# Kernel optimization log

Measured on AMD Instinct MI355X. Metric: run time of the kernel, lower is better.

Reference implementation:

```python
import jax, jax.numpy as jnp
import numpy as np

E, T, K, H, I = 16, 512, 8, 2048, 1024  # experts, tokens, top-k, hidden, ffn half-width


def setup_inputs() -> dict:
    key = jax.random.key(0)
    ks = jax.random.split(key, 8)
    x = jax.random.normal(ks[0], (T, H), dtype=jnp.float32)
    expert_ids = jax.random.randint(ks[1], (T, K), 0, E, dtype=jnp.int32)
    # int8-valued weights stored as int32 (exactly representable)
    gmm1_weight = jax.random.randint(ks[2], (E, H, 2 * I), -127, 128, dtype=jnp.int32)
    gmm2_weight = jax.random.randint(ks[3], (E, I, H), -127, 128, dtype=jnp.int32)
    gmm1_weight_scale = jax.random.uniform(ks[4], (E, 2 * I), dtype=jnp.float32) * 1e-3
    gmm2_weight_scale = jax.random.uniform(ks[5], (E, H), dtype=jnp.float32) * 1e-3
    smooth_scales = jax.random.uniform(ks[6], (E, H), dtype=jnp.float32)
    expert_scales = jax.random.uniform(ks[7], (T, K), dtype=jnp.float32)
    return {"x": x, "expert_ids": expert_ids, "gmm1_weight": gmm1_weight,
            "gmm1_weight_scale": gmm1_weight_scale, "gmm2_weight": gmm2_weight,
            "gmm2_weight_scale": gmm2_weight_scale, "smooth_scales": smooth_scales,
            "expert_scales": expert_scales}


def _dynamic_quant(v):
    # per-token symmetric dynamic quant to int8 range (quant_mode=2 / quant_mode=1)
    s = jnp.max(jnp.abs(v), axis=-1, keepdims=True) / 127.0
    q = jnp.clip(jnp.round(v / s), -128.0, 127.0)  # kept in f32; values are exact small ints
    return q, s


def _grouped_mm(a, w, e_flat):
    # grouped GEMM: out[i] = a[i] @ w[e_flat[i]]. Disjoint expert masks -> masked full GEMMs summed.
    out = jnp.zeros((a.shape[0], w.shape[-1]), dtype=a.dtype)
    for e in range(w.shape[0]):
        mask = (e_flat == e)[:, None]
        out = out + jnp.where(mask, a, 0.0) @ w[e]
    return out


def reference(x, expert_ids, gmm1_weight, gmm1_weight_scale, gmm2_weight,
              gmm2_weight_scale, smooth_scales, expert_scales):
    # --- dispatch: per-token dynamic int8 quant + replicate each token K times ---
    xq, s0 = _dynamic_quant(x)                 # [T,H], [T,1]
    e_flat = expert_ids.reshape(-1)            # [T*K]
    xq_e = jnp.repeat(xq, K, axis=0)           # [T*K,H]
    s0_e = jnp.repeat(s0, K, axis=0)           # [T*K,1] == dynamic_scales / activation_scale
    w1 = gmm1_weight.astype(jnp.float32)       # int8 GEMM emulated exactly in f32
    w2 = gmm2_weight.astype(jnp.float32)
    # --- grouped GEMM 1 -> int32 accumulator values ---
    y1_i32 = _grouped_mm(xq_e, w1, e_flat)     # [T*K,2I]
    # --- fused dequant + SwiGLU (activate_left) + per-token dynamic requant ---
    y1f = y1_i32 * gmm1_weight_scale[e_flat] * s0_e
    act = jax.nn.silu(y1f[:, :I]) * y1f[:, I:]
    aq, s1 = _dynamic_quant(act)               # [T*K,I], [T*K,1]
    # --- grouped GEMM 2 + dequant (per-channel weight scale * per-token scale) ---
    y2_i32 = _grouped_mm(aq, w2, e_flat)       # [T*K,H]
    y2 = y2_i32 * gmm2_weight_scale[e_flat] * s1
    # --- combine: weighted sum over the K expert copies of each token ---
    out = jnp.einsum('tkh,tk->th', y2.reshape(T, K, H), expert_scales)
    return out
```

## Files before the change

kernel.cpp:

```cpp
#include <hip/hip_runtime.h>
#include <hip/hip_bf16.h>
#include <stdint.h>

#define E_   16
#define T_   512
#define KTOP 8
#define H_   2048
#define I_   1024
#define TK_  4096

typedef __attribute__((ext_vector_type(4))) int i32x4;

#define OFF_CNT     0
#define OFF_ROWMAX  4096
#define OFF_XQ      32768
#define OFF_S0      (OFF_XQ + T_*H_)
#define OFF_S1      (OFF_S0 + 4096)
#define OFF_LIST    (OFF_S1 + TK_*4)
#define OFF_ACT     (OFF_LIST + E_*TK_*4)
#define OFF_AQ      (OFF_ACT + (size_t)TK_*I_*4)
#define OFF_Y2      (OFF_AQ + (size_t)TK_*I_)

__device__ __forceinline__ void g2l16(const void* g, void* l) {
  __builtin_amdgcn_global_load_lds(
      (const __attribute__((address_space(1))) void*)g,
      (__attribute__((address_space(3))) void*)l, 16, 0, 0);
}

#define SCHEDB() __builtin_amdgcn_sched_barrier(0)
#define VMCNT16() asm volatile("s_waitcnt vmcnt(16)" ::: "memory")
#define VMCNT0()  asm volatile("s_waitcnt vmcnt(0)" ::: "memory")
#define LGKM0()   asm volatile("s_waitcnt lgkmcnt(0)" ::: "memory")
#define BAR()     __builtin_amdgcn_s_barrier()

__global__ void k_zero(unsigned int* __restrict__ p) {
  int i = blockIdx.x * 256 + threadIdx.x;
  if (i < 5120) p[i] = 0;
}

__global__ void k_quant(const float* __restrict__ x, signed char* __restrict__ xq,
                        float* __restrict__ s0, const int* __restrict__ eids,
                        unsigned int* __restrict__ counts, int* __restrict__ row_list) {
  int t = blockIdx.x, tid = threadIdx.x;
  if (tid < KTOP) {
    int e = eids[t * KTOP + tid];
    int pos = (int)atomicAdd(&counts[e], 1u);
    row_list[e * TK_ + pos] = t * KTOP + tid;
  }
  const float4* xr = (const float4*)(x + (size_t)t * H_);
  float4 a = xr[tid * 2 + 0], b = xr[tid * 2 + 1];
  float m = fmaxf(
      fmaxf(fmaxf(fabsf(a.x), fabsf(a.y)), fmaxf(fabsf(a.z), fabsf(a.w))),
      fmaxf(fmaxf(fabsf(b.x), fabsf(b.y)), fmaxf(fabsf(b.z), fabsf(b.w))));
  for (int o = 32; o > 0; o >>= 1) m = fmaxf(m, __shfl_xor(m, o));
  __shared__ float wm[4];
  if ((tid & 63) == 0) wm[tid >> 6] = m;
  __syncthreads();
  m = fmaxf(fmaxf(wm[0], wm[1]), fmaxf(wm[2], wm[3]));
  float s = m / 127.0f;
  if (!(s > 0.f)) s = 1.0f;
  if (tid == 0) s0[t] = s;
  float v[8] = {a.x, a.y, a.z, a.w, b.x, b.y, b.z, b.w};
  unsigned int lo = 0, hi = 0;
#pragma unroll
  for (int j = 0; j < 4; ++j) {
    float qf = fminf(fmaxf(rintf(v[j] / s), -128.f), 127.f);
    lo |= ((unsigned)((int)qf & 0xFF)) << (8 * j);
  }
#pragma unroll
  for (int j = 0; j < 4; ++j) {
    float qf = fminf(fmaxf(rintf(v[4 + j] / s), -128.f), 127.f);
    hi |= ((unsigned)((int)qf & 0xFF)) << (8 * j);
  }
  ((uint2*)(xq + (size_t)t * H_))[tid] = make_uint2(lo, hi);
}

#define BM_   320
#define ABUF  20480
#define BBUF  4096
#define WSTR  2048

#define PACKW(SRC, DST) do {                                              \
    i32x4 pk_;                                                            \
    _Pragma("unroll")                                                     \
    for (int d_ = 0; d_ < 4; ++d_)                                        \
      pk_[d_] = ((SRC)[4*d_] & 0xFF) | (((SRC)[4*d_+1] & 0xFF) << 8) |    \
                (((SRC)[4*d_+2] & 0xFF) << 16) | ((SRC)[4*d_+3] << 24);   \
    *(i32x4*)(DST) = pk_;                                                 \
  } while (0)

#define TILE_BODY(TT, RD, PK, IS, LAST, NT) do {                          \
    if (!(LAST)) {                                                        \
      _Pragma("unroll")                                                   \
      for (int i_ = 0; i_ < 5; ++i_)                                      \
        g2l16(gA[i_] + ((TT) + 1) * 64,                                   \
              smem + ((RD) ^ 1) * ABUF + (w * 5 + i_) * 1024);            \
    }                                                                     \
    SCHEDB();                                                             \
    {                                                                     \
      int kk_ = (TT) + 2; if (kk_ > (NT) - 1) kk_ = (NT) - 1;             \
      _Pragma("unroll")                                                   \
      for (int j_ = 0; j_ < 16; ++j_)                                     \
        (IS)[j_] = bsrc[(size_t)(kk_ * 64 + j_) * WSTR];                  \
    }                                                                     \
    SCHEDB();                                                             \
    {                                                                     \
      const char* Ab_ = smem + (RD) * ABUF;                               \
      const char* Bb_ = smem + 2 * ABUF + (RD) * BBUF;                    \
      i32x4 af_[5], bf_[4];                                               \
      _Pragma("unroll")                                                   \
      for (int i_ = 0; i_ < 5; ++i_)                                      \
        af_[i_] = *(const i32x4*)(Ab_ + (w * 5 + i_) * 1024 + lane * 16); \
      _Pragma("unroll")                                                   \
      for (int n_ = 0; n_ < 4; ++n_)                                      \
        bf_[n_] = *(const i32x4*)(Bb_ + l4 * 1024 + (n_ * 16 + l15) * 16);\
      _Pragma("unroll")                                                   \
      for (int i_ = 0; i_ < 5; ++i_)                                      \
        _Pragma("unroll")                                                 \
        for (int n_ = 0; n_ < 4; ++n_)                                    \
          acc[i_][n_] = __builtin_amdgcn_mfma_i32_16x16x64_i8(            \
              af_[i_], bf_[n_], acc[i_][n_], 0, 0, 0);                    \
    }                                                                     \
    if (!(LAST)) {                                                        \
      VMCNT16(); SCHEDB();                                                \
      PACKW(PK, bdst0 + (((RD) ^ 1)) * BBUF);                             \
      LGKM0(); BAR(); SCHEDB();                                           \
    }                                                                     \
  } while (0)

__launch_bounds__(256, 2)
__global__ void k_gemm1(const signed char* __restrict__ xq, const int* __restrict__ w1,
                        const float* __restrict__ ws1, const float* __restrict__ s0,
                        const unsigned int* __restrict__ counts,
                        const int* __restrict__ row_list,
                        float* __restrict__ act, unsigned int* __restrict__ rowmax) {
  __shared__ alignas(16) char smem[2 * ABUF + 2 * BBUF];
  int e = blockIdx.y;
  int cnt = (int)counts[e];
  if (cnt == 0) return;
  int p0 = blockIdx.x * 32;
  const int* rl = row_list + e * TK_;
  const int* we = w1 + (size_t)e * H_ * (2 * I_);
  const float* wsc = ws1 + (size_t)e * (2 * I_);

  int tid = threadIdx.x, w = tid >> 6, lane = tid & 63;
  int l15 = lane & 15, l4 = lane >> 4;
  int bc = tid & 63, bkg = tid >> 6;
  int bgcol = (bc < 32) ? (p0 + bc) : (I_ + p0 + (bc - 32));
  const int* bsrc = we + (size_t)(bkg * 16) * WSTR + bgcol;
  char* bdst0 = smem + 2 * ABUF + bkg * 1024 + bc * 16;

  const int NT = H_ / 64;
  int nch = (cnt + BM_ - 1) / BM_;
  for (int ch = 0; ch < nch; ++ch) {
    int rbase = ch * BM_;
    const signed char* gA[5];
#pragma unroll
    for (int i = 0; i < 5; ++i) {
      int gr = rbase + w * 80 + i * 16 + l15;
      int tok = rl[gr < cnt ? gr : 0] >> 3;
      gA[i] = xq + (size_t)tok * H_ + l4 * 16;
    }
    i32x4 acc[5][4];
#pragma unroll
    for (int i = 0; i < 5; ++i)
#pragma unroll
      for (int n = 0; n < 4; ++n) acc[i][n] = (i32x4)(0);

    int brA[16], brB[16];
    SCHEDB();
#pragma unroll
    for (int i = 0; i < 5; ++i) g2l16(gA[i], smem + (w * 5 + i) * 1024);
    SCHEDB();
#pragma unroll
    for (int j = 0; j < 16; ++j) brA[j] = bsrc[(size_t)j * WSTR];
    SCHEDB();
#pragma unroll
    for (int j = 0; j < 16; ++j) brB[j] = bsrc[(size_t)(64 + j) * WSTR];
    SCHEDB();
    VMCNT16(); SCHEDB();
    PACKW(brA, bdst0);
    LGKM0(); BAR(); SCHEDB();

    for (int t = 0; t < NT; t += 2) {
      TILE_BODY(t,     0, brB, brA, false,          NT);
      TILE_BODY(t + 1, 1, brA, brB, (t + 2 == NT),  NT);
    }

#pragma unroll
    for (int mi = 0; mi < 5; ++mi) {
#pragma unroll
      for (int r = 0; r < 4; ++r) {
        int gr = rbase + w * 80 + mi * 16 + l4 * 4 + r;
        bool valid = gr < cnt;
        int irow = rl[valid ? gr : 0];
        float s0v = s0[irow >> 3];
        float rowm = 0.f, av0 = 0.f, av1 = 0.f;
#pragma unroll
        for (int n = 0; n < 2; ++n) {
          int colL = p0 + n * 16 + l15;
          float yl = (float)acc[mi][n][r] * wsc[colL] * s0v;
          float yr = (float)acc[mi][n + 2][r] * wsc[I_ + colL] * s0v;
          float actv = (yl / (1.f + expf(-yl))) * yr;
          if (n == 0) av0 = actv; else av1 = actv;
          rowm = fmaxf(rowm, fabsf(actv));
        }
        rowm = fmaxf(rowm, __shfl_xor(rowm, 1));
        rowm = fmaxf(rowm, __shfl_xor(rowm, 2));
        rowm = fmaxf(rowm, __shfl_xor(rowm, 4));
        rowm = fmaxf(rowm, __shfl_xor(rowm, 8));
        if (valid) {
          act[(size_t)irow * I_ + p0 + l15] = av0;
          act[(size_t)irow * I_ + p0 + 16 + l15] = av1;
          if (l15 == 0) atomicMax(rowmax + irow, __float_as_uint(rowm));
        }
      }
    }
  }
}

__global__ void k_requant(const float* __restrict__ act, const unsigned int* __restrict__ rowmax,
                          signed char* __restrict__ aq, float* __restrict__ s1) {
  int i = blockIdx.x, tid = threadIdx.x;
  float m = __uint_as_float(rowmax[i]);
  float s = (m > 0.f) ? (m / 127.0f) : 1.0f;
  if (tid == 0) s1[i] = s;
  float4 v = ((const float4*)(act + (size_t)i * I_))[tid];
  float vv[4] = {v.x, v.y, v.z, v.w};
  unsigned int pk = 0;
#pragma unroll
  for (int j = 0; j < 4; ++j) {
    float qf = fminf(fmaxf(rintf(vv[j] / s), -128.f), 127.f);
    pk |= ((unsigned)((int)qf & 0xFF)) << (8 * j);
  }
  ((unsigned int*)(aq + (size_t)i * I_))[tid] = pk;
}

__launch_bounds__(256, 2)
__global__ void k_gemm2(const signed char* __restrict__ aq, const int* __restrict__ w2,
                        const float* __restrict__ ws2, const float* __restrict__ s1,
                        const float* __restrict__ es,
                        const unsigned int* __restrict__ counts,
                        const int* __restrict__ row_list,
                        __hip_bfloat16* __restrict__ y2h) {
  __shared__ alignas(16) char smem[2 * ABUF + 2 * BBUF];
  int e = blockIdx.y;
  int cnt = (int)counts[e];
  if (cnt == 0) return;
  int n0 = blockIdx.x * 64;
  const int* rl = row_list + e * TK_;
  const int* we = w2 + (size_t)e * I_ * H_;
  const float* wsc = ws2 + (size_t)e * H_;

  int tid = threadIdx.x, w = tid >> 6, lane = tid & 63;
  int l15 = lane & 15, l4 = lane >> 4;
  int bc = tid & 63, bkg = tid >> 6;
  const int* bsrc = we + (size_t)(bkg * 16) * WSTR + n0 + bc;
  char* bdst0 = smem + 2 * ABUF + bkg * 1024 + bc * 16;

  const int NT = I_ / 64;
  int nch = (cnt + BM_ - 1) / BM_;
  for (int ch = 0; ch < nch; ++ch) {
    int rbase = ch * BM_;
    const signed char* gA[5];
#pragma unroll
    for (int i = 0; i < 5; ++i) {
      int gr = rbase + w * 80 + i * 16 + l15;
      gA[i] = aq + (size_t)rl[gr < cnt ? gr : 0] * I_ + l4 * 16;
    }
    i32x4 acc[5][4];
#pragma unroll
    for (int i = 0; i < 5; ++i)
#pragma unroll
      for (int n = 0; n < 4; ++n) acc[i][n] = (i32x4)(0);

    int brA[16], brB[16];
    SCHEDB();
#pragma unroll
    for (int i = 0; i < 5; ++i) g2l16(gA[i], smem + (w * 5 + i) * 1024);
    SCHEDB();
#pragma unroll
    for (int j = 0; j < 16; ++j) brA[j] = bsrc[(size_t)j * WSTR];
    SCHEDB();
#pragma unroll
    for (int j = 0; j < 16; ++j) brB[j] = bsrc[(size_t)(64 + j) * WSTR];
    SCHEDB();
    VMCNT16(); SCHEDB();
    PACKW(brA, bdst0);
    LGKM0(); BAR(); SCHEDB();

    for (int t = 0; t < NT; t += 2) {
      TILE_BODY(t,     0, brB, brA, false,          NT);
      TILE_BODY(t + 1, 1, brA, brB, (t + 2 == NT),  NT);
    }

#pragma unroll
    for (int mi = 0; mi < 5; ++mi) {
#pragma unroll
      for (int r = 0; r < 4; ++r) {
        int gr = rbase + w * 80 + mi * 16 + l4 * 4 + r;
        if (gr < cnt) {
          int irow = rl[gr];
          float sc = s1[irow] * es[irow];
#pragma unroll
          for (int n = 0; n < 4; ++n) {
            int col = n0 + n * 16 + l15;
            float v = (float)acc[mi][n][r] * wsc[col] * sc;
            y2h[(size_t)irow * H_ + col] = __float2bfloat16(v);
          }
        }
      }
    }
  }
}

__global__ void k_combine(const __hip_bfloat16* __restrict__ y2h, float* __restrict__ out) {
  int idx = blockIdx.x * 256 + threadIdx.x;
  int t = idx >> 8;
  int h0 = (idx & 255) * 8;
  float s[8];
#pragma unroll
  for (int j = 0; j < 8; ++j) s[j] = 0.f;
#pragma unroll
  for (int k = 0; k < KTOP; ++k) {
    const __hip_bfloat16* p = y2h + ((size_t)(t * KTOP + k) * H_ + h0);
    uint4 u = *(const uint4*)p;
    const __hip_bfloat16* b = (const __hip_bfloat16*)&u;
#pragma unroll
    for (int j = 0; j < 8; ++j) s[j] += __bfloat162float(b[j]);
  }
  float4 o0 = make_float4(s[0], s[1], s[2], s[3]);
  float4 o1 = make_float4(s[4], s[5], s[6], s[7]);
  float4* dst = (float4*)(out + (size_t)t * H_ + h0);
  dst[0] = o0; dst[1] = o1;
}

extern "C" void kernel_launch(void* const* d_in, const int* in_sizes, int n_in,
                              void* d_out, int out_size, void* d_ws, size_t ws_size,
                              hipStream_t stream) {
  const float* x   = (const float*)d_in[0];
  const int*   eid = (const int*)d_in[1];
  const int*   w1  = (const int*)d_in[2];
  const float* ws1 = (const float*)d_in[3];
  const int*   w2  = (const int*)d_in[4];
  const float* ws2 = (const float*)d_in[5];
  const float* es  = (const float*)d_in[7];
  float* out = (float*)d_out;
  char* ws = (char*)d_ws;

  unsigned int*  counts   = (unsigned int*)(ws + OFF_CNT);
  unsigned int*  rowmax   = (unsigned int*)(ws + OFF_ROWMAX);
  signed char*   xq       = (signed char*)(ws + OFF_XQ);
  float*         s0       = (float*)(ws + OFF_S0);
  float*         s1       = (float*)(ws + OFF_S1);
  int*           row_list = (int*)(ws + OFF_LIST);
  float*         act      = (float*)(ws + OFF_ACT);
  signed char*   aq       = (signed char*)(ws + OFF_AQ);
  __hip_bfloat16* y2h     = (__hip_bfloat16*)(ws + OFF_Y2);

  k_zero<<<20, 256, 0, stream>>>((unsigned int*)ws);
  k_quant<<<T_, 256, 0, stream>>>(x, xq, s0, eid, counts, row_list);
  k_gemm1<<<dim3(32, E_), 256, 0, stream>>>(xq, w1, ws1, s0, counts, row_list, act, rowmax);
  k_requant<<<TK_, 256, 0, stream>>>(act, rowmax, aq, s1);
  k_gemm2<<<dim3(32, E_), 256, 0, stream>>>(aq, w2, ws2, s1, es, counts, row_list, y2h);
  k_combine<<<(T_ * H_ / 8) / 256, 256, 0, stream>>>(y2h, out);
}
```

Baseline: 178.2 us.

## Replace LDS-staged GEMM blocks with single-wave register-pipelined tiles over more blocks

Both grouped GEMM kernels drop the 256-thread LDS double-buffered design. They now use 64-thread single-wave blocks that load A and B fragments straight into registers with a two-stage register double buffer. The grid gains a third dimension that splits row chunks across 5 blocks, and each block covers a narrower column strip (16+16 columns for gemm1, 32 for gemm2), giving many more blocks to fill the GPU. The cost is weaker reuse: each weight column strip is reloaded by more blocks, B is fetched with strided scalar int32 loads per wave, and there is no shared-memory sharing.

```diff
diff --git a/kernel.cpp b/kernel.cpp
--- a/kernel.cpp
+++ b/kernel.cpp
@@ -20,18 +20,6 @@
 #define OFF_ACT     (OFF_LIST + E_*TK_*4)
 #define OFF_AQ      (OFF_ACT + (size_t)TK_*I_*4)
 #define OFF_Y2      (OFF_AQ + (size_t)TK_*I_)
-
-__device__ __forceinline__ void g2l16(const void* g, void* l) {
-  __builtin_amdgcn_global_load_lds(
-      (const __attribute__((address_space(1))) void*)g,
-      (__attribute__((address_space(3))) void*)l, 16, 0, 0);
-}
-
-#define SCHEDB() __builtin_amdgcn_sched_barrier(0)
-#define VMCNT16() asm volatile("s_waitcnt vmcnt(16)" ::: "memory")
-#define VMCNT0()  asm volatile("s_waitcnt vmcnt(0)" ::: "memory")
-#define LGKM0()   asm volatile("s_waitcnt lgkmcnt(0)" ::: "memory")
-#define BAR()     __builtin_amdgcn_s_barrier()
 
 __global__ void k_zero(unsigned int* __restrict__ p) {
   int i = blockIdx.x * 256 + threadIdx.x;
@@ -75,143 +63,105 @@
   ((uint2*)(xq + (size_t)t * H_))[tid] = make_uint2(lo, hi);
 }
 
-#define BM_   320
-#define ABUF  20480
-#define BBUF  4096
-#define WSTR  2048
-
-#define PACKW(SRC, DST) do {                                              \
-    i32x4 pk_;                                                            \
+__device__ __forceinline__ i32x4 packb(const int* s) {
+  i32x4 r;
+#pragma unroll
+  for (int d = 0; d < 4; ++d)
+    r[d] = (s[4 * d] & 0xFF) | ((s[4 * d + 1] & 0xFF) << 8) |
+           ((s[4 * d + 2] & 0xFF) << 16) | (s[4 * d + 3] << 24);
+  return r;
+}
+
+#define LOADA(BANK, TT)                                                   \
+  _Pragma("unroll")                                                       \
+  for (int i_ = 0; i_ < 5; ++i_)                                          \
+    BANK[i_] = *(const i32x4*)(gA[i_] + (TT) * 64);
+
+#define LOADB(BL, BR, TT)                                                 \
+  _Pragma("unroll")                                                       \
+  for (int j_ = 0; j_ < 16; ++j_) {                                       \
+    BL[j_] = weL[(size_t)((TT) * 64 + j_) * 2048];                        \
+    BR[j_] = weR[(size_t)((TT) * 64 + j_) * 2048];                        \
+  }
+
+#define COMP(AB, BL, BR)                                                  \
+  do {                                                                    \
+    i32x4 fL_ = packb(BL), fR_ = packb(BR);                               \
     _Pragma("unroll")                                                     \
-    for (int d_ = 0; d_ < 4; ++d_)                                        \
-      pk_[d_] = ((SRC)[4*d_] & 0xFF) | (((SRC)[4*d_+1] & 0xFF) << 8) |    \
-                (((SRC)[4*d_+2] & 0xFF) << 16) | ((SRC)[4*d_+3] << 24);   \
-    *(i32x4*)(DST) = pk_;                                                 \
-  } while (0)
-
-#define TILE_BODY(TT, RD, PK, IS, LAST, NT) do {                          \
-    if (!(LAST)) {                                                        \
-      _Pragma("unroll")                                                   \
-      for (int i_ = 0; i_ < 5; ++i_)                                      \
-        g2l16(gA[i_] + ((TT) + 1) * 64,                                   \
-              smem + ((RD) ^ 1) * ABUF + (w * 5 + i_) * 1024);            \
-    }                                                                     \
-    SCHEDB();                                                             \
-    {                                                                     \
-      int kk_ = (TT) + 2; if (kk_ > (NT) - 1) kk_ = (NT) - 1;             \
-      _Pragma("unroll")                                                   \
-      for (int j_ = 0; j_ < 16; ++j_)                                     \
-        (IS)[j_] = bsrc[(size_t)(kk_ * 64 + j_) * WSTR];                  \
-    }                                                                     \
-    SCHEDB();                                                             \
-    {                                                                     \
-      const char* Ab_ = smem + (RD) * ABUF;                               \
-      const char* Bb_ = smem + 2 * ABUF + (RD) * BBUF;                    \
-      i32x4 af_[5], bf_[4];                                               \
-      _Pragma("unroll")                                                   \
-      for (int i_ = 0; i_ < 5; ++i_)                                      \
-        af_[i_] = *(const i32x4*)(Ab_ + (w * 5 + i_) * 1024 + lane * 16); \
-      _Pragma("unroll")                                                   \
-      for (int n_ = 0; n_ < 4; ++n_)                                      \
-        bf_[n_] = *(const i32x4*)(Bb_ + l4 * 1024 + (n_ * 16 + l15) * 16);\
-      _Pragma("unroll")                                                   \
-      for (int i_ = 0; i_ < 5; ++i_)                                      \
-        _Pragma("unroll")                                                 \
-        for (int n_ = 0; n_ < 4; ++n_)                                    \
-          acc[i_][n_] = __builtin_amdgcn_mfma_i32_16x16x64_i8(            \
-              af_[i_], bf_[n_], acc[i_][n_], 0, 0, 0);                    \
-    }                                                                     \
-    if (!(LAST)) {                                                        \
-      VMCNT16(); SCHEDB();                                                \
-      PACKW(PK, bdst0 + (((RD) ^ 1)) * BBUF);                             \
-      LGKM0(); BAR(); SCHEDB();                                           \
+    for (int i_ = 0; i_ < 5; ++i_) {                                      \
+      acc[i_][0] = __builtin_amdgcn_mfma_i32_16x16x64_i8(                 \
+          AB[i_], fL_, acc[i_][0], 0, 0, 0);                              \
+      acc[i_][1] = __builtin_amdgcn_mfma_i32_16x16x64_i8(                 \
+          AB[i_], fR_, acc[i_][1], 0, 0, 0);                              \
     }                                                                     \
   } while (0)
 
-__launch_bounds__(256, 2)
+__launch_bounds__(64, 2)
 __global__ void k_gemm1(const signed char* __restrict__ xq, const int* __restrict__ w1,
                         const float* __restrict__ ws1, const float* __restrict__ s0,
                         const unsigned int* __restrict__ counts,
                         const int* __restrict__ row_list,
                         float* __restrict__ act, unsigned int* __restrict__ rowmax) {
-  __shared__ alignas(16) char smem[2 * ABUF + 2 * BBUF];
+  int strip = blockIdx.x;
   int e = blockIdx.y;
   int cnt = (int)counts[e];
-  if (cnt == 0) return;
-  int p0 = blockIdx.x * 32;
+  int p0 = strip * 16;
   const int* rl = row_list + e * TK_;
   const int* we = w1 + (size_t)e * H_ * (2 * I_);
   const float* wsc = ws1 + (size_t)e * (2 * I_);
 
-  int tid = threadIdx.x, w = tid >> 6, lane = tid & 63;
+  int lane = threadIdx.x & 63;
   int l15 = lane & 15, l4 = lane >> 4;
-  int bc = tid & 63, bkg = tid >> 6;
-  int bgcol = (bc < 32) ? (p0 + bc) : (I_ + p0 + (bc - 32));
-  const int* bsrc = we + (size_t)(bkg * 16) * WSTR + bgcol;
-  char* bdst0 = smem + 2 * ABUF + bkg * 1024 + bc * 16;
-
-  const int NT = H_ / 64;
-  int nch = (cnt + BM_ - 1) / BM_;
-  for (int ch = 0; ch < nch; ++ch) {
-    int rbase = ch * BM_;
+
+  const int* weL = we + (size_t)(l4 * 16) * 2048 + p0 + l15;
+  const int* weR = weL + I_;
+
+  for (int ch = blockIdx.z; ch * 80 < cnt; ch += 5) {
+    int rbase = ch * 80;
     const signed char* gA[5];
 #pragma unroll
     for (int i = 0; i < 5; ++i) {
-      int gr = rbase + w * 80 + i * 16 + l15;
+      int gr = rbase + i * 16 + l15;
       int tok = rl[gr < cnt ? gr : 0] >> 3;
       gA[i] = xq + (size_t)tok * H_ + l4 * 16;
     }
-    i32x4 acc[5][4];
-#pragma unroll
-    for (int i = 0; i < 5; ++i)
-#pragma unroll
-      for (int n = 0; n < 4; ++n) acc[i][n] = (i32x4)(0);
-
-    int brA[16], brB[16];
-    SCHEDB();
-#pragma unroll
-    for (int i = 0; i < 5; ++i) g2l16(gA[i], smem + (w * 5 + i) * 1024);
-    SCHEDB();
-#pragma unroll
-    for (int j = 0; j < 16; ++j) brA[j] = bsrc[(size_t)j * WSTR];
-    SCHEDB();
-#pragma unroll
-    for (int j = 0; j < 16; ++j) brB[j] = bsrc[(size_t)(64 + j) * WSTR];
-    SCHEDB();
-    VMCNT16(); SCHEDB();
-    PACKW(brA, bdst0);
-    LGKM0(); BAR(); SCHEDB();
-
-    for (int t = 0; t < NT; t += 2) {
-      TILE_BODY(t,     0, brB, brA, false,          NT);
-      TILE_BODY(t + 1, 1, brA, brB, (t + 2 == NT),  NT);
+    i32x4 acc[5][2];
+#pragma unroll
+    for (int i = 0; i < 5; ++i) { acc[i][0] = (i32x4)(0); acc[i][1] = (i32x4)(0); }
+
+    i32x4 a0[5], a1[5];
+    int b0L[16], b0R[16], b1L[16], b1R[16];
+
+    LOADA(a0, 0);
+    LOADB(b0L, b0R, 0);
+    for (int t = 0; t < 32; t += 2) {
+      LOADA(a1, t + 1);
+      LOADB(b1L, b1R, t + 1);
+      COMP(a0, b0L, b0R);
+      int p2 = (t + 2 < 32) ? (t + 2) : t;
+      LOADA(a0, p2);
+      LOADB(b0L, b0R, p2);
+      COMP(a1, b1L, b1R);
     }
 
 #pragma unroll
     for (int mi = 0; mi < 5; ++mi) {
 #pragma unroll
       for (int r = 0; r < 4; ++r) {
-        int gr = rbase + w * 80 + mi * 16 + l4 * 4 + r;
+        int gr = rbase + mi * 16 + l4 * 4 + r;
         bool valid = gr < cnt;
         int irow = rl[valid ? gr : 0];
         float s0v = s0[irow >> 3];
-        float rowm = 0.f, av0 = 0.f, av1 = 0.f;
-#pragma unroll
-        for (int n = 0; n < 2; ++n) {
-          int colL = p0 + n * 16 + l15;
-          float yl = (float)acc[mi][n][r] * wsc[colL] * s0v;
-          float yr = (float)acc[mi][n + 2][r] * wsc[I_ + colL] * s0v;
-          float actv = (yl / (1.f + expf(-yl))) * yr;
-          if (n == 0) av0 = actv; else av1 = actv;
-          rowm = fmaxf(rowm, fabsf(actv));
-        }
+        float yl = (float)acc[mi][0][r] * wsc[p0 + l15] * s0v;
+        float yr = (float)acc[mi][1][r] * wsc[I_ + p0 + l15] * s0v;
+        float actv = (yl / (1.f + expf(-yl))) * yr;
+        float rowm = fabsf(actv);
         rowm = fmaxf(rowm, __shfl_xor(rowm, 1));
         rowm = fmaxf(rowm, __shfl_xor(rowm, 2));
         rowm = fmaxf(rowm, __shfl_xor(rowm, 4));
         rowm = fmaxf(rowm, __shfl_xor(rowm, 8));
         if (valid) {
-          act[(size_t)irow * I_ + p0 + l15] = av0;
-          act[(size_t)irow * I_ + p0 + 16 + l15] = av1;
+          act[(size_t)irow * I_ + p0 + l15] = actv;
           if (l15 == 0) atomicMax(rowmax + irow, __float_as_uint(rowm));
         }
       }
@@ -236,77 +186,67 @@
   ((unsigned int*)(aq + (size_t)i * I_))[tid] = pk;
 }
 
-__launch_bounds__(256, 2)
+__launch_bounds__(64, 2)
 __global__ void k_gemm2(const signed char* __restrict__ aq, const int* __restrict__ w2,
                         const float* __restrict__ ws2, const float* __restrict__ s1,
                         const float* __restrict__ es,
                         const unsigned int* __restrict__ counts,
                         const int* __restrict__ row_list,
                         __hip_bfloat16* __restrict__ y2h) {
-  __shared__ alignas(16) char smem[2 * ABUF + 2 * BBUF];
+  int strip = blockIdx.x;
   int e = blockIdx.y;
   int cnt = (int)counts[e];
-  if (cnt == 0) return;
-  int n0 = blockIdx.x * 64;
+  int n0 = strip * 32;
   const int* rl = row_list + e * TK_;
   const int* we = w2 + (size_t)e * I_ * H_;
   const float* wsc = ws2 + (size_t)e * H_;
 
-  int tid = threadIdx.x, w = tid >> 6, lane = tid & 63;
+  int lane = threadIdx.x & 63;
   int l15 = lane & 15, l4 = lane >> 4;
-  int bc = tid & 63, bkg = tid >> 6;
-  const int* bsrc = we + (size_t)(bkg * 16) * WSTR + n0 + bc;
-  char* bdst0 = smem + 2 * ABUF + bkg * 1024 + bc * 16;
-
-  const int NT = I_ / 64;
-  int nch = (cnt + BM_ - 1) / BM_;
-  for (int ch = 0; ch < nch; ++ch) {
-    int rbase = ch * BM_;
+
+  const int* weL = we + (size_t)(l4 * 16) * 2048 + n0 + l15;
+  const int* weR = weL + 16;
+
+  for (int ch = blockIdx.z; ch * 80 < cnt; ch += 5) {
+    int rbase = ch * 80;
     const signed char* gA[5];
 #pragma unroll
     for (int i = 0; i < 5; ++i) {
-      int gr = rbase + w * 80 + i * 16 + l15;
+      int gr = rbase + i * 16 + l15;
       gA[i] = aq + (size_t)rl[gr < cnt ? gr : 0] * I_ + l4 * 16;
     }
-    i32x4 acc[5][4];
-#pragma unroll
-    for (int i = 0; i < 5; ++i)
-#pragma unroll
-      for (int n = 0; n < 4; ++n) acc[i][n] = (i32x4)(0);
-
-    int brA[16], brB[16];
-    SCHEDB();
-#pragma unroll
-    for (int i = 0; i < 5; ++i) g2l16(gA[i], smem + (w * 5 + i) * 1024);
-    SCHEDB();
-#pragma unroll
-    for (int j = 0; j < 16; ++j) brA[j] = bsrc[(size_t)j * WSTR];
-    SCHEDB();
-#pragma unroll
-    for (int j = 0; j < 16; ++j) brB[j] = bsrc[(size_t)(64 + j) * WSTR];
-    SCHEDB();
-    VMCNT16(); SCHEDB();
-    PACKW(brA, bdst0);
-    LGKM0(); BAR(); SCHEDB();
-
-    for (int t = 0; t < NT; t += 2) {
-      TILE_BODY(t,     0, brB, brA, false,          NT);
-      TILE_BODY(t + 1, 1, brA, brB, (t + 2 == NT),  NT);
+    i32x4 acc[5][2];
+#pragma unroll
+    for (int i = 0; i < 5; ++i) { acc[i][0] = (i32x4)(0); acc[i][1] = (i32x4)(0); }
+
+    i32x4 a0[5], a1[5];
+    int b0L[16], b0R[16], b1L[16], b1R[16];
+
+    LOADA(a0, 0);
+    LOADB(b0L, b0R, 0);
+    for (int t = 0; t < 16; t += 2) {
+      LOADA(a1, t + 1);
+      LOADB(b1L, b1R, t + 1);
+      COMP(a0, b0L, b0R);
+      int p2 = (t + 2 < 16) ? (t + 2) : t;
+      LOADA(a0, p2);
+      LOADB(b0L, b0R, p2);
+      COMP(a1, b1L, b1R);
     }
 
 #pragma unroll
     for (int mi = 0; mi < 5; ++mi) {
 #pragma unroll
       for (int r = 0; r < 4; ++r) {
-        int gr = rbase + w * 80 + mi * 16 + l4 * 4 + r;
+        int gr = rbase + mi * 16 + l4 * 4 + r;
         if (gr < cnt) {
           int irow = rl[gr];
           float sc = s1[irow] * es[irow];
 #pragma unroll
-          for (int n = 0; n < 4; ++n) {
-            int col = n0 + n * 16 + l15;
-            float v = (float)acc[mi][n][r] * wsc[col] * sc;
-            y2h[(size_t)irow * H_ + col] = __float2bfloat16(v);
+          for (int n = 0; n < 2; ++n) {
+            int c = n0 + n * 16 + l15;
+            float v = (float)acc[mi][n][r] * wsc[c] * sc;
+            y2h[(size_t)irow * H_ + c] = __float2bfloat16(v);
           }
         }
       }
@@ -360,8 +300,8 @@
 
   k_zero<<<20, 256, 0, stream>>>((unsigned int*)ws);
   k_quant<<<T_, 256, 0, stream>>>(x, xq, s0, eid, counts, row_list);
-  k_gemm1<<<dim3(32, E_), 256, 0, stream>>>(xq, w1, ws1, s0, counts, row_list, act, rowmax);
+  k_gemm1<<<dim3(64, E_, 5), 64, 0, stream>>>(xq, w1, ws1, s0, counts, row_list, act, rowmax);
   k_requant<<<TK_, 256, 0, stream>>>(act, rowmax, aq, s1);
-  k_gemm2<<<dim3(32, E_), 256, 0, stream>>>(aq, w2, ws2, s1, es, counts, row_list, y2h);
+  k_gemm2<<<dim3(64, E_, 5), 64, 0, stream>>>(aq, w2, ws2, s1, es, counts, row_list, y2h);
   k_combine<<<(T_ * H_ / 8) / 256, 256, 0, stream>>>(y2h, out);
 }
```

After: 456.4 us. 2.56x slower.

## Load A tiles directly into registers, stage only B through LDS

Applied to the files above, without the earlier changes.

Both grouped GEMM kernels now load the activation (A) fragments straight from global memory into registers, double-buffered across k-tiles, instead of staging them through LDS with global_load_lds. Only the packed weight (B) tile still goes through a small double-buffered LDS area, which cuts shared memory per block from about 48KB to 8KB. This removes the LDS write/read round trip for A. In exchange it adds register pressure from the extra A and B register banks, makes global A loads lane-gathered rather than LDS-mediated, and needs a barrier between row chunks.

```diff
diff --git a/kernel.cpp b/kernel.cpp
--- a/kernel.cpp
+++ b/kernel.cpp
@@ -21,15 +21,8 @@
 #define OFF_AQ      (OFF_ACT + (size_t)TK_*I_*4)
 #define OFF_Y2      (OFF_AQ + (size_t)TK_*I_)
 
-__device__ __forceinline__ void g2l16(const void* g, void* l) {
-  __builtin_amdgcn_global_load_lds(
-      (const __attribute__((address_space(1))) void*)g,
-      (__attribute__((address_space(3))) void*)l, 16, 0, 0);
-}
-
 #define SCHEDB() __builtin_amdgcn_sched_barrier(0)
-#define VMCNT16() asm volatile("s_waitcnt vmcnt(16)" ::: "memory")
-#define VMCNT0()  asm volatile("s_waitcnt vmcnt(0)" ::: "memory")
+#define VMCNT26() asm volatile("s_waitcnt vmcnt(26)" ::: "memory")
 #define LGKM0()   asm volatile("s_waitcnt lgkmcnt(0)" ::: "memory")
 #define BAR()     __builtin_amdgcn_s_barrier()
 
@@ -76,8 +69,6 @@
 }
 
 #define BM_   320
-#define ABUF  20480
-#define BBUF  4096
 #define WSTR  2048
 
 #define PACKW(SRC, DST) do {                                              \
@@ -89,41 +80,39 @@
     *(i32x4*)(DST) = pk_;                                                 \
   } while (0)
 
-#define TILE_BODY(TT, RD, PK, IS, LAST, NT) do {                          \
-    if (!(LAST)) {                                                        \
+#define LOADB(BANK, TT)                                                   \
+    _Pragma("unroll")                                                     \
+    for (int j_ = 0; j_ < 16; ++j_)                                       \
+      BANK[j_] = bsrc[(size_t)((TT) * 64 + j_) * WSTR];
+
+#define LOADAR(BANK, TT)                                                  \
+    _Pragma("unroll")                                                     \
+    for (int i_ = 0; i_ < 5; ++i_)                                        \
+      BANK[i_] = *(const i32x4*)(gA[i_] + (TT) * 64);
+
+#define MFMAS(ABANK, P)                                                   \
+    _Pragma("unroll")                                                     \
+    for (int n_ = 0; n_ < 4; ++n_) {                                      \
+      i32x4 bf_ = *(const i32x4*)(bsm + (P) * 4096 + l4 * 1024 +          \
+                                  (n_ * 16 + l15) * 16);                  \
       _Pragma("unroll")                                                   \
       for (int i_ = 0; i_ < 5; ++i_)                                      \
-        g2l16(gA[i_] + ((TT) + 1) * 64,                                   \
-              smem + ((RD) ^ 1) * ABUF + (w * 5 + i_) * 1024);            \
-    }                                                                     \
+        acc[i_][n_] = __builtin_amdgcn_mfma_i32_16x16x64_i8(              \
+            ABANK[i_], bf_, acc[i_][n_], 0, 0, 0);                        \
+    }
+
+#define TILE(TT, P, ABANK, BBANK, PKBANK, NT, LAST) do {                  \
+    int tn_ = (TT) + 2; if (tn_ > (NT) - 1) tn_ = (NT) - 1;               \
     SCHEDB();                                                             \
-    {                                                                     \
-      int kk_ = (TT) + 2; if (kk_ > (NT) - 1) kk_ = (NT) - 1;             \
-      _Pragma("unroll")                                                   \
-      for (int j_ = 0; j_ < 16; ++j_)                                     \
-        (IS)[j_] = bsrc[(size_t)(kk_ * 64 + j_) * WSTR];                  \
-    }                                                                     \
+    LOADB(BBANK, tn_);                                                    \
     SCHEDB();                                                             \
-    {                                                                     \
-      const char* Ab_ = smem + (RD) * ABUF;                               \
-      const char* Bb_ = smem + 2 * ABUF + (RD) * BBUF;                    \
-      i32x4 af_[5], bf_[4];                                               \
-      _Pragma("unroll")                                                   \
-      for (int i_ = 0; i_ < 5; ++i_)                                      \
-        af_[i_] = *(const i32x4*)(Ab_ + (w * 5 + i_) * 1024 + lane * 16); \
-      _Pragma("unroll")                                                   \
-      for (int n_ = 0; n_ < 4; ++n_)                                      \
-        bf_[n_] = *(const i32x4*)(Bb_ + l4 * 1024 + (n_ * 16 + l15) * 16);\
-      _Pragma("unroll")                                                   \
-      for (int i_ = 0; i_ < 5; ++i_)                                      \
-        _Pragma("unroll")                                                 \
-        for (int n_ = 0; n_ < 4; ++n_)                                    \
-          acc[i_][n_] = __builtin_amdgcn_mfma_i32_16x16x64_i8(            \
-              af_[i_], bf_[n_], acc[i_][n_], 0, 0, 0);                    \
-    }                                                                     \
+    MFMAS(ABANK, P);                                                      \
+    SCHEDB();                                                             \
+    LOADAR(ABANK, tn_);                                                   \
+    SCHEDB();                                                             \
     if (!(LAST)) {                                                        \
-      VMCNT16(); SCHEDB();                                                \
-      PACKW(PK, bdst0 + (((RD) ^ 1)) * BBUF);                             \
+      VMCNT26(); SCHEDB();                                                \
+      PACKW(PKBANK, bsm + ((P) ^ 1) * 4096 + bkg * 1024 + bc * 16);       \
       LGKM0(); BAR(); SCHEDB();                                           \
     }                                                                     \
   } while (0)
@@ -134,7 +123,7 @@
                         const unsigned int* __restrict__ counts,
                         const int* __restrict__ row_list,
                         float* __restrict__ act, unsigned int* __restrict__ rowmax) {
-  __shared__ alignas(16) char smem[2 * ABUF + 2 * BBUF];
+  __shared__ alignas(16) char bsm[2 * 4096];
   int e = blockIdx.y;
   int cnt = (int)counts[e];
   if (cnt == 0) return;
@@ -148,11 +137,11 @@
   int bc = tid & 63, bkg = tid >> 6;
   int bgcol = (bc < 32) ? (p0 + bc) : (I_ + p0 + (bc - 32));
   const int* bsrc = we + (size_t)(bkg * 16) * WSTR + bgcol;
-  char* bdst0 = smem + 2 * ABUF + bkg * 1024 + bc * 16;
 
   const int NT = H_ / 64;
   int nch = (cnt + BM_ - 1) / BM_;
   for (int ch = 0; ch < nch; ++ch) {
+    if (ch) { BAR(); }
     int rbase = ch * BM_;
     const signed char* gA[5];
 #pragma unroll
@@ -167,24 +156,23 @@
 #pragma unroll
       for (int n = 0; n < 4; ++n) acc[i][n] = (i32x4)(0);
 
-    int brA[16], brB[16];
-    SCHEDB();
-#pragma unroll
-    for (int i = 0; i < 5; ++i) g2l16(gA[i], smem + (w * 5 + i) * 1024);
-    SCHEDB();
-#pragma unroll
-    for (int j = 0; j < 16; ++j) brA[j] = bsrc[(size_t)j * WSTR];
-    SCHEDB();
-#pragma unroll
-    for (int j = 0; j < 16; ++j) brB[j] = bsrc[(size_t)(64 + j) * WSTR];
-    SCHEDB();
-    VMCNT16(); SCHEDB();
-    PACKW(brA, bdst0);
+    i32x4 aR0[5], aR1[5];
+    int bR0[16], bR1[16];
+    SCHEDB();
+    LOADB(bR0, 0);
+    SCHEDB();
+    LOADAR(aR0, 0);
+    LOADAR(aR1, 1);
+    SCHEDB();
+    LOADB(bR1, 1);
+    SCHEDB();
+    VMCNT26(); SCHEDB();
+    PACKW(bR0, bsm + bkg * 1024 + bc * 16);
     LGKM0(); BAR(); SCHEDB();
 
     for (int t = 0; t < NT; t += 2) {
-      TILE_BODY(t,     0, brB, brA, false,          NT);
-      TILE_BODY(t + 1, 1, brA, brB, (t + 2 == NT),  NT);
+      TILE(t,     0, aR0, bR0, bR1, NT, false);
+      TILE(t + 1, 1, aR1, bR1, bR0, NT, (t + 2 >= NT));
     }
 
 #pragma unroll
@@ -243,7 +231,7 @@
                         const unsigned int* __restrict__ counts,
                         const int* __restrict__ row_list,
                         __hip_bfloat16* __restrict__ y2h) {
-  __shared__ alignas(16) char smem[2 * ABUF + 2 * BBUF];
+  __shared__ alignas(16) char bsm[2 * 4096];
   int e = blockIdx.y;
   int cnt = (int)counts[e];
   if (cnt == 0) return;
@@ -256,11 +244,11 @@
   int l15 = lane & 15, l4 = lane >> 4;
   int bc = tid & 63, bkg = tid >> 6;
   const int* bsrc = we + (size_t)(bkg * 16) * WSTR + n0 + bc;
-  char* bdst0 = smem + 2 * ABUF + bkg * 1024 + bc * 16;
 
   const int NT = I_ / 64;
   int nch = (cnt + BM_ - 1) / BM_;
   for (int ch = 0; ch < nch; ++ch) {
+    if (ch) { BAR(); }
     int rbase = ch * BM_;
     const signed char* gA[5];
 #pragma unroll
@@ -274,24 +262,23 @@
 #pragma unroll
       for (int n = 0; n < 4; ++n) acc[i][n] = (i32x4)(0);
 
-    int brA[16], brB[16];
-    SCHEDB();
-#pragma unroll
-    for (int i = 0; i < 5; ++i) g2l16(gA[i], smem + (w * 5 + i) * 1024);
-    SCHEDB();
-#pragma unroll
-    for (int j = 0; j < 16; ++j) brA[j] = bsrc[(size_t)j * WSTR];
-    SCHEDB();
-#pragma unroll
-    for (int j = 0; j < 16; ++j) brB[j] = bsrc[(size_t)(64 + j) * WSTR];
-    SCHEDB();
-    VMCNT16(); SCHEDB();
-    PACKW(brA, bdst0);
+    i32x4 aR0[5], aR1[5];
+    int bR0[16], bR1[16];
+    SCHEDB();
+    LOADB(bR0, 0);
+    SCHEDB();
+    LOADAR(aR0, 0);
+    LOADAR(aR1, 1);
+    SCHEDB();
+    LOADB(bR1, 1);
+    SCHEDB();
+    VMCNT26(); SCHEDB();
+    PACKW(bR0, bsm + bkg * 1024 + bc * 16);
     LGKM0(); BAR(); SCHEDB();
 
     for (int t = 0; t < NT; t += 2) {
-      TILE_BODY(t,     0, brB, brA, false,          NT);
-      TILE_BODY(t + 1, 1, brA, brB, (t + 2 == NT),  NT);
+      TILE(t,     0, aR0, bR0, bR1, NT, false);
+      TILE(t + 1, 1, aR1, bR1, bR0, NT, (t + 2 >= NT));
     }
 
 #pragma unroll
@@ -304,9 +291,9 @@
           float sc = s1[irow] * es[irow];
 #pragma unroll
           for (int n = 0; n < 4; ++n) {
-            int col = n0 + n * 16 + l15;
-            float v = (float)acc[mi][n][r] * wsc[col] * sc;
-            y2h[(size_t)irow * H_ + col] = __float2bfloat16(v);
+            int c = n0 + n * 16 + l15;
+            float v = (float)acc[mi][n][r] * wsc[c] * sc;
+            y2h[(size_t)irow * H_ + c] = __float2bfloat16(v);
           }
         }
       }
```

New measurement: 183.4 us. 1.03x slower.
